# Kernel tuning notes

Hardware: AMD Instinct MI355X
Metric: run time of the kernel (lower is better)

The kernel has to match this reference:

```python
import jax, jax.numpy as jnp
import numpy as np
from jax import lax

TAGSET_SIZE = 64
START_TAG = TAGSET_SIZE - 2
STOP_TAG = TAGSET_SIZE - 1
NEG_INF = -10000.0


def setup_inputs() -> dict:
    key = jax.random.key(0)
    k_feat, k_trans, k_tags = jax.random.split(key, 3)
    B, S, T = 512, 1024, TAGSET_SIZE
    feats = jax.random.normal(k_feat, (B, S, T), dtype=jnp.float32)
    transitions = jax.random.normal(k_trans, (T, T), dtype=jnp.float32)
    # CRF constraints: nothing transitions FROM anything into START row semantics
    # of the torch code: transitions[START, :] = -1e4 ; transitions[:, STOP] = -1e4
    transitions = transitions.at[START_TAG, :].set(NEG_INF)
    transitions = transitions.at[:, STOP_TAG].set(NEG_INF)
    tags = jax.random.randint(k_tags, (B, S), 0, T - 2, dtype=jnp.int64)
    mask = jnp.ones((B, S), dtype=jnp.int32)
    return {"feats": feats, "transitions": transitions, "tags": tags, "mask": mask}


def _forward_alg(feats, transitions, maskf):
    # feats: (B,S,T), maskf: (B,S) float
    B, S, T = feats.shape
    init = jnp.full((B, T), NEG_INF, dtype=feats.dtype).at[:, START_TAG].set(0.0)

    def step(fv, xs):
        feat, m = xs  # feat: (B,T), m: (B,)
        # next_tag_var[b, next, prev] = fv[b,prev] + trans[next,prev] + feat[b,next]
        nxt = jax.nn.logsumexp(
            fv[:, None, :] + transitions[None, :, :] + feat[:, :, None], axis=2
        )
        m1 = m[:, None]
        return nxt * m1 + fv * (1.0 - m1), None

    fv, _ = lax.scan(step, init, (feats.transpose(1, 0, 2), maskf.T))
    terminal = fv + transitions[STOP_TAG][None, :]
    return jax.nn.logsumexp(terminal, axis=1)  # (B,)


def _score_sentence(feats, transitions, tags, maskf):
    B, S, T = feats.shape
    tags_ext = jnp.concatenate(
        [jnp.full((B, 1), START_TAG, dtype=tags.dtype), tags], axis=1
    )  # (B, S+1)
    cur = tags_ext[:, 1:]   # (B,S)
    prev = tags_ext[:, :-1]  # (B,S)
    emit = jnp.take_along_axis(feats, cur[:, :, None], axis=2)[:, :, 0]  # (B,S)
    trans = transitions[cur, prev]  # (B,S)
    score = jnp.sum((emit + trans) * maskf, axis=1)
    last_idx = maskf.sum(axis=1).astype(jnp.int32)  # index into tags_ext
    last_tags = jnp.take_along_axis(tags_ext, last_idx[:, None].astype(tags.dtype), axis=1)[:, 0]
    return score + transitions[STOP_TAG, last_tags]


def reference(feats, transitions, tags, mask):
    maskf = mask.astype(feats.dtype)
    forward_score = _forward_alg(feats, transitions, maskf)
    gold_score = _score_sentence(feats, transitions, tags, maskf)
    return jnp.mean(forward_score - gold_score)
```

## Files before the change

### kernel.cpp

```cpp
#include <hip/hip_runtime.h>

#define START_TAG 62
#define STOP_TAG 63
#define BATCH 512
#define SLEN 1024
#define NG 32
#define NCHAIN 64
#define RD 12
#define AH 8
#define SLOTB 4096
#define RINGB (RD * SLOTB)

typedef float vf4 __attribute__((ext_vector_type(4)));
typedef short short8 __attribute__((ext_vector_type(8)));

__device__ __forceinline__ unsigned pk_bf16(float lo, float hi) {
  return __builtin_amdgcn_perm(__float_as_uint(hi), __float_as_uint(lo), 0x07060302u);
}
__device__ __forceinline__ short bf16_rne(float x) {
  unsigned u = __float_as_uint(x);
  u += 0x7FFFu + ((u >> 16) & 1u);
  return (short)(u >> 16);
}
__device__ __forceinline__ vf4 mfma16(short8 a, short8 b, vf4 c) {
  return __builtin_amdgcn_mfma_f32_16x16x32_bf16(a, b, c, 0, 0, 0);
}
__device__ __forceinline__ void async16(const void* g, void* l) {
  __builtin_amdgcn_global_load_lds((const __attribute__((address_space(1))) unsigned*)g,
                                   (__attribute__((address_space(3))) unsigned*)l, 16, 0, 0);
}

template<int DIR, bool MASKED>
__device__ __forceinline__ void chain_run(const float* __restrict__ feats,
                                          const float* __restrict__ trans,
                                          const int* __restrict__ mask,
                                          float* __restrict__ ws, char* smem, int g) {
  const int lane = threadIdx.x & 63;
  const int q = lane >> 4, col = lane & 15;
  const int b = g * 16 + col;

  short8 A[4][2];
  const int mrow = 16 * (col >> 2) + (col & 3);
  #pragma unroll
  for (int t = 0; t < 4; ++t) {
    #pragma unroll
    for (int c = 0; c < 2; ++c) {
      short8 a;
      #pragma unroll
      for (int j = 0; j < 8; ++j) {
        int R = mrow + 4 * t, K = 16 * q + 8 * c + j;
        float tv = (DIR == 0) ? trans[R * 64 + K] : trans[K * 64 + R];
        a[j] = bf16_rne(__expf(tv));
      }
      A[t][c] = a;
    }
  }

  float W[16];
  float C = 0.f;
  if (DIR == 0) {
    #pragma unroll
    for (int i = 0; i < 16; ++i) W[i] = 0.f;
    if (q == 3) W[14] = 1.f;
  } else {
    #pragma unroll
    for (int i = 0; i < 16; ++i) W[i] = __expf(trans[STOP_TAG * 64 + 16 * q + i]);
  }

  const char* gb = (const char*)feats + (size_t)b * 262144 + (size_t)q * 64;

  vf4 cur[4];
  int rOff = 0, wOff = 0;
  if constexpr (!MASKED) {
    asm volatile("s_waitcnt vmcnt(0)" ::: "memory");
    #pragma unroll
    for (int p = 0; p < AH; ++p) {
      int s = (DIR == 0) ? p : 1023 - p;
      #pragma unroll
      for (int v = 0; v < 4; ++v)
        async16(gb + (size_t)s * 256 + v * 16, smem + p * SLOTB + v * 1024);
    }
    wOff = AH * SLOTB;
    asm volatile("s_waitcnt vmcnt(28)" ::: "memory");
    #pragma unroll
    for (int v = 0; v < 4; ++v)
      cur[v] = *(const vf4*)(smem + v * 1024 + lane * 16);
    rOff = SLOTB;
  } else {
    int s0 = (DIR == 0) ? 0 : 1023;
    #pragma unroll
    for (int v = 0; v < 4; ++v)
      cur[v] = *(const vf4*)(gb + (size_t)s0 * 256 + v * 16);
  }

  for (int grp = 0; grp < 128; ++grp) {
    #pragma unroll
    for (int u = 0; u < 4; ++u) {
      const int j = grp * 4 + u;
      float e[16];
      #pragma unroll
      for (int v = 0; v < 4; ++v)
        #pragma unroll
        for (int i = 0; i < 4; ++i) e[v * 4 + i] = __expf(cur[v][i]);

      float P[16];
      #pragma unroll
      for (int i = 0; i < 16; ++i) P[i] = (DIR == 0) ? W[i] : W[i] * e[i];

      union { unsigned uu[4]; short8 s8; } B0, B1;
      B0.uu[0] = pk_bf16(P[0], P[1]);   B0.uu[1] = pk_bf16(P[2], P[3]);
      B0.uu[2] = pk_bf16(P[4], P[5]);   B0.uu[3] = pk_bf16(P[6], P[7]);
      B1.uu[0] = pk_bf16(P[8], P[9]);   B1.uu[1] = pk_bf16(P[10], P[11]);
      B1.uu[2] = pk_bf16(P[12], P[13]); B1.uu[3] = pk_bf16(P[14], P[15]);

      vf4 z4 = {0.f, 0.f, 0.f, 0.f};
      vf4 d0 = mfma16(A[0][0], B0.s8, z4);
      vf4 d1 = mfma16(A[1][0], B0.s8, z4);
      vf4 d2 = mfma16(A[2][0], B0.s8, z4);
      vf4 d3 = mfma16(A[3][0], B0.s8, z4);
      d0 = mfma16(A[0][1], B1.s8, d0);
      d1 = mfma16(A[1][1], B1.s8, d1);
      d2 = mfma16(A[2][1], B1.s8, d2);
      d3 = mfma16(A[3][1], B1.s8, d3);

      int m = 1;
      if constexpr (!MASKED) {
        asm volatile("s_waitcnt vmcnt(24)" ::: "memory");
        #pragma unroll
        for (int v = 0; v < 4; ++v)
          cur[v] = *(const vf4*)(smem + rOff + v * 1024 + lane * 16);
        rOff += SLOTB; if (rOff == RINGB) rOff = 0;
        int jp = j + AH; if (jp > 511) jp = 511;
        int sp = (DIR == 0) ? jp : 1023 - jp;
        #pragma unroll
        for (int v = 0; v < 4; ++v)
          async16(gb + (size_t)sp * 256 + v * 16, smem + wOff + v * 1024);
        wOff += SLOTB; if (wOff == RINGB) wOff = 0;
      } else {
        int sj = (DIR == 0) ? j : 1023 - j;
        m = mask[b * 1024 + sj];
        int sn = (DIR == 0) ? (j + 1) : 1023 - (j + 1);
        #pragma unroll
        for (int v = 0; v < 4; ++v)
          cur[v] = *(const vf4*)(gb + (size_t)sn * 256 + v * 16);
      }

      #pragma unroll
      for (int i = 0; i < 4; ++i) {
        float n0 = (DIR == 0) ? d0[i] * e[i]      : d0[i];
        float n1 = (DIR == 0) ? d1[i] * e[4 + i]  : d1[i];
        float n2 = (DIR == 0) ? d2[i] * e[8 + i]  : d2[i];
        float n3 = (DIR == 0) ? d3[i] * e[12 + i] : d3[i];
        if (MASKED) {
          W[i]      = m ? n0 : W[i];
          W[4 + i]  = m ? n1 : W[4 + i];
          W[8 + i]  = m ? n2 : W[8 + i];
          W[12 + i] = m ? n3 : W[12 + i];
        } else {
          W[i] = n0; W[4 + i] = n1; W[8 + i] = n2; W[12 + i] = n3;
        }
      }
    }
    float z = __shfl(W[0], col);
    float rz = __builtin_amdgcn_rcpf(z);
    C += __logf(z);
    #pragma unroll
    for (int i = 0; i < 16; ++i) W[i] *= rz;
  }

  float* slab = ws + (size_t)(g * 2 + DIR) * 1024;
  #pragma unroll
  for (int t4 = 0; t4 < 4; ++t4) {
    vf4 o = {W[t4 * 4], W[t4 * 4 + 1], W[t4 * 4 + 2], W[t4 * 4 + 3]};
    *(vf4*)(slab + lane * 16 + t4 * 4) = o;
  }
  if (q == 0) ws[65536 + (g * 2 + DIR) * 16 + col] = C;
}

__global__ __launch_bounds__(64, 1)
void crf_main(const float* __restrict__ feats, const float* __restrict__ trans,
              const int* __restrict__ tags, const int* __restrict__ mask,
              float* __restrict__ ws) {
  __shared__ char smem[RINGB];
  const int blk = blockIdx.x;
  if (blk < NCHAIN) {
    const int g = blk >> 1, dir = blk & 1;
    const int lane = threadIdx.x & 63;
    const int q = lane >> 4, col = lane & 15;
    const int b = g * 16 + col;
    const int sB = dir ? 512 : 0;
    int anyz = 0;
    for (int it = 0; it < 32; ++it) {
      int4 v = *(const int4*)(mask + b * 1024 + sB + (it * 4 + q) * 4);
      anyz |= (v.x == 0) | (v.y == 0) | (v.z == 0) | (v.w == 0);
    }
    bool allones = (__ballot(anyz != 0) == 0ull);
    if (allones) {
      if (dir == 0) chain_run<0, false>(feats, trans, mask, ws, smem, g);
      else          chain_run<1, false>(feats, trans, mask, ws, smem, g);
    } else {
      if (dir == 0) chain_run<0, true>(feats, trans, mask, ws, smem, g);
      else          chain_run<1, true>(feats, trans, mask, ws, smem, g);
    }
    (void)tags;
  } else {
    const int b = blk - NCHAIN;
    const int* tb = tags + b * SLEN;
    const int* mb = mask + b * SLEN;
    const float* fbg = feats + (size_t)b * 65536;
    float acc = 0.f, cnt = 0.f;
    const int t = threadIdx.x;
    for (int k = 0; k < 16; ++k) {
      int s = t + k * 64;
      int cur = tb[s];
      int prev = (s == 0) ? START_TAG : tb[s - 1];
      float m = (float)mb[s];
      acc += m * (fbg[s * 64 + cur] + trans[cur * 64 + prev]);
      cnt += m;
    }
    #pragma unroll
    for (int o = 1; o < 64; o <<= 1) {
      acc += __shfl_xor(acc, o);
      cnt += __shfl_xor(cnt, o);
    }
    if (t == 0) {
      int last_idx = (int)(cnt + 0.5f);
      int last_tag = (last_idx == 0) ? START_TAG : tb[last_idx - 1];
      ws[66560 + b] = acc + trans[STOP_TAG * 64 + last_tag];
    }
  }
}

__global__ __launch_bounds__(512)
void crf_reduce(const float* __restrict__ ws, float* __restrict__ out) {
  __shared__ float s[512];
  const int t = threadIdx.x;
  const int g = t >> 4, col = t & 15;
  const float* Wf = ws + (size_t)(2 * g) * 1024;
  const float* Wb = ws + (size_t)(2 * g + 1) * 1024;
  float P = 0.f;
  #pragma unroll
  for (int q = 0; q < 4; ++q)
    #pragma unroll
    for (int i = 0; i < 16; ++i)
      P += Wf[(q * 16 + col) * 16 + i] * Wb[(q * 16 + col) * 16 + i];
  float sc = ws[65536 + (2 * g) * 16 + col] + ws[65536 + (2 * g + 1) * 16 + col] + __logf(P);
  s[t] = sc - ws[66560 + t];
  __syncthreads();
  for (int off = 256; off > 0; off >>= 1) {
    if (t < off) s[t] += s[t + off];
    __syncthreads();
  }
  if (t == 0) out[0] = s[0] * (1.f / 512.f);
}

extern "C" void kernel_launch(void* const* d_in, const int* in_sizes, int n_in,
                              void* d_out, int out_size, void* d_ws, size_t ws_size,
                              hipStream_t stream) {
  const float* feats = (const float*)d_in[0];
  const float* trans = (const float*)d_in[1];
  const int* tags = (const int*)d_in[2];
  const int* mask = (const int*)d_in[3];
  float* ws = (float*)d_ws;
  float* out = (float*)d_out;

  crf_main<<<NCHAIN + BATCH, 64, 0, stream>>>(feats, trans, tags, mask, ws);
  crf_reduce<<<1, 512, 0, stream>>>(ws, out);
}
```

Before: 309.6 us.

## Restructure fast CRF chain with 16-slot ring, compile-time slots, deferred renormalization

Splits the chain kernel into separate unmasked-fast and masked paths. The fast path now uses a 16-slot LDS ring, which lets a 16-step unrolled loop use compile-time slot indices instead of runtime offset arithmetic. Each async prefetch is issued before its matching wait, and the next step's LDS read happens early. Renormalization runs every 4 steps using a scale value captured one interval earlier, which takes the cross-lane shuffle off the critical dependency chain. The cost is more LDS per block and a deferred scale that lets values grow slightly more between rescales.

```diff
diff --git a/kernel.cpp b/kernel.cpp
--- a/kernel.cpp
+++ b/kernel.cpp
@@ -4,12 +4,10 @@
 #define STOP_TAG 63
 #define BATCH 512
 #define SLEN 1024
-#define NG 32
 #define NCHAIN 64
-#define RD 12
+#define RD 16
 #define AH 8
 #define SLOTB 4096
-#define RINGB (RD * SLOTB)
 
 typedef float vf4 __attribute__((ext_vector_type(4)));
 typedef short short8 __attribute__((ext_vector_type(8)));
@@ -30,16 +28,9 @@
                                    (__attribute__((address_space(3))) unsigned*)l, 16, 0, 0);
 }
 
-template<int DIR, bool MASKED>
-__device__ __forceinline__ void chain_run(const float* __restrict__ feats,
-                                          const float* __restrict__ trans,
-                                          const int* __restrict__ mask,
-                                          float* __restrict__ ws, char* smem, int g) {
-  const int lane = threadIdx.x & 63;
-  const int q = lane >> 4, col = lane & 15;
-  const int b = g * 16 + col;
-
-  short8 A[4][2];
+template<int DIR>
+__device__ __forceinline__ void load_A(const float* __restrict__ trans, short8 A[4][2],
+                                       int q, int col) {
   const int mrow = 16 * (col >> 2) + (col & 3);
   #pragma unroll
   for (int t = 0; t < 4; ++t) {
@@ -55,9 +46,32 @@
       A[t][c] = a;
     }
   }
+}
+
+template<int DIR>
+__device__ __forceinline__ void epilogue(float* __restrict__ ws, const float W[16],
+                                         float C, int g, int lane, int q, int col) {
+  float* slab = ws + (size_t)(g * 2 + DIR) * 1024;
+  #pragma unroll
+  for (int t4 = 0; t4 < 4; ++t4) {
+    vf4 o = {W[t4 * 4], W[t4 * 4 + 1], W[t4 * 4 + 2], W[t4 * 4 + 3]};
+    *(vf4*)(slab + lane * 16 + t4 * 4) = o;
+  }
+  if (q == 0) ws[65536 + (g * 2 + DIR) * 16 + col] = C;
+}
+
+template<int DIR>
+__device__ __forceinline__ void chain_fast(const float* __restrict__ feats,
+                                           const float* __restrict__ trans,
+                                           float* __restrict__ ws, char* smem, int g) {
+  const int lane = threadIdx.x & 63;
+  const int q = lane >> 4, col = lane & 15;
+  const int b = g * 16 + col;
+
+  short8 A[4][2];
+  load_A<DIR>(trans, A, q, col);
 
   float W[16];
-  float C = 0.f;
   if (DIR == 0) {
     #pragma unroll
     for (int i = 0; i < 16; ++i) W[i] = 0.f;
@@ -69,34 +83,39 @@
 
   const char* gb = (const char*)feats + (size_t)b * 262144 + (size_t)q * 64;
 
+  asm volatile("s_waitcnt vmcnt(0)" ::: "memory");
+  #pragma unroll
+  for (int p = 0; p < AH; ++p) {
+    size_t s = (DIR == 0) ? (size_t)p : (size_t)(1023 - p);
+    #pragma unroll
+    for (int v = 0; v < 4; ++v)
+      async16(gb + s * 256 + v * 16, smem + p * SLOTB + v * 1024);
+  }
+  asm volatile("s_waitcnt vmcnt(28)" ::: "memory");
   vf4 cur[4];
-  int rOff = 0, wOff = 0;
-  if constexpr (!MASKED) {
-    asm volatile("s_waitcnt vmcnt(0)" ::: "memory");
-    #pragma unroll
-    for (int p = 0; p < AH; ++p) {
-      int s = (DIR == 0) ? p : 1023 - p;
-      #pragma unroll
-      for (int v = 0; v < 4; ++v)
-        async16(gb + (size_t)s * 256 + v * 16, smem + p * SLOTB + v * 1024);
-    }
-    wOff = AH * SLOTB;
-    asm volatile("s_waitcnt vmcnt(28)" ::: "memory");
-    #pragma unroll
-    for (int v = 0; v < 4; ++v)
-      cur[v] = *(const vf4*)(smem + v * 1024 + lane * 16);
-    rOff = SLOTB;
-  } else {
-    int s0 = (DIR == 0) ? 0 : 1023;
-    #pragma unroll
-    for (int v = 0; v < 4; ++v)
-      cur[v] = *(const vf4*)(gb + (size_t)s0 * 256 + v * 16);
-  }
-
-  for (int grp = 0; grp < 128; ++grp) {
-    #pragma unroll
-    for (int u = 0; u < 4; ++u) {
-      const int j = grp * 4 + u;
+  #pragma unroll
+  for (int v = 0; v < 4; ++v)
+    cur[v] = *(const vf4*)(smem + v * 1024 + lane * 16);
+
+  float C = 0.f, zpend = 1.f;
+
+  for (int bk = 0; bk < 32; ++bk) {
+    #pragma unroll
+    for (int u = 0; u < 16; ++u) {
+      const int j = bk * 16 + u;
+      int jp = j + AH; if (jp > 511) jp = 511;
+      const size_t sp = (DIR == 0) ? (size_t)jp : (size_t)(1023 - jp);
+      const int wslot = (u + AH) & 15;
+      #pragma unroll
+      for (int v = 0; v < 4; ++v)
+        async16(gb + sp * 256 + v * 16, smem + wslot * SLOTB + v * 1024);
+      asm volatile("s_waitcnt vmcnt(28)" ::: "memory");
+      const int rslot = (u + 1) & 15;
+      vf4 nxt[4];
+      #pragma unroll
+      for (int v = 0; v < 4; ++v)
+        nxt[v] = *(const vf4*)(smem + rslot * SLOTB + v * 1024 + lane * 16);
+
       float e[16];
       #pragma unroll
       for (int v = 0; v < 4; ++v)
@@ -123,27 +142,96 @@
       d2 = mfma16(A[2][1], B1.s8, d2);
       d3 = mfma16(A[3][1], B1.s8, d3);
 
-      int m = 1;
-      if constexpr (!MASKED) {
-        asm volatile("s_waitcnt vmcnt(24)" ::: "memory");
+      #pragma unroll
+      for (int i = 0; i < 4; ++i) {
+        W[i]      = (DIR == 0) ? d0[i] * e[i]      : d0[i];
+        W[4 + i]  = (DIR == 0) ? d1[i] * e[4 + i]  : d1[i];
+        W[8 + i]  = (DIR == 0) ? d2[i] * e[8 + i]  : d2[i];
+        W[12 + i] = (DIR == 0) ? d3[i] * e[12 + i] : d3[i];
+      }
+      #pragma unroll
+      for (int v = 0; v < 4; ++v) cur[v] = nxt[v];
+
+      if ((u & 3) == 3) {
+        float rz = __builtin_amdgcn_rcpf(zpend);
+        C += __logf(zpend);
         #pragma unroll
-        for (int v = 0; v < 4; ++v)
-          cur[v] = *(const vf4*)(smem + rOff + v * 1024 + lane * 16);
-        rOff += SLOTB; if (rOff == RINGB) rOff = 0;
-        int jp = j + AH; if (jp > 511) jp = 511;
-        int sp = (DIR == 0) ? jp : 1023 - jp;
+        for (int i = 0; i < 16; ++i) W[i] *= rz;
+        zpend = __shfl(W[0], col);
+      }
+    }
+  }
+  epilogue<DIR>(ws, W, C, g, lane, q, col);
+}
+
+template<int DIR>
+__device__ __forceinline__ void chain_masked(const float* __restrict__ feats,
+                                             const float* __restrict__ trans,
+                                             const int* __restrict__ mask,
+                                             float* __restrict__ ws, int g) {
+  const int lane = threadIdx.x & 63;
+  const int q = lane >> 4, col = lane & 15;
+  const int b = g * 16 + col;
+
+  short8 A[4][2];
+  load_A<DIR>(trans, A, q, col);
+
+  float W[16];
+  float C = 0.f;
+  if (DIR == 0) {
+    #pragma unroll
+    for (int i = 0; i < 16; ++i) W[i] = 0.f;
+    if (q == 3) W[14] = 1.f;
+  } else {
+    #pragma unroll
+    for (int i = 0; i < 16; ++i) W[i] = __expf(trans[STOP_TAG * 64 + 16 * q + i]);
+  }
+
+  const char* gb = (const char*)feats + (size_t)b * 262144 + (size_t)q * 64;
+  vf4 cur[4];
+  {
+    size_t s0 = (DIR == 0) ? 0 : 1023;
+    #pragma unroll
+    for (int v = 0; v < 4; ++v)
+      cur[v] = *(const vf4*)(gb + s0 * 256 + (size_t)v * 16);
+  }
+
+  for (int grp = 0; grp < 128; ++grp) {
+    #pragma unroll
+    for (int u = 0; u < 4; ++u) {
+      const int j = grp * 4 + u;
+      float e[16];
+      #pragma unroll
+      for (int v = 0; v < 4; ++v)
         #pragma unroll
-        for (int v = 0; v < 4; ++v)
-          async16(gb + (size_t)sp * 256 + v * 16, smem + wOff + v * 1024);
-        wOff += SLOTB; if (wOff == RINGB) wOff = 0;
-      } else {
-        int sj = (DIR == 0) ? j : 1023 - j;
-        m = mask[b * 1024 + sj];
-        int sn = (DIR == 0) ? (j + 1) : 1023 - (j + 1);
-        #pragma unroll
-        for (int v = 0; v < 4; ++v)
-          cur[v] = *(const vf4*)(gb + (size_t)sn * 256 + v * 16);
-      }
+        for (int i = 0; i < 4; ++i) e[v * 4 + i] = __expf(cur[v][i]);
+
+      float P[16];
+      #pragma unroll
+      for (int i = 0; i < 16; ++i) P[i] = (DIR == 0) ? W[i] : W[i] * e[i];
+
+      union { unsigned uu[4]; short8 s8; } B0, B1;
+      B0.uu[0] = pk_bf16(P[0], P[1]);   B0.uu[1] = pk_bf16(P[2], P[3]);
+      B0.uu[2] = pk_bf16(P[4], P[5]);   B0.uu[3] = pk_bf16(P[6], P[7]);
+      B1.uu[0] = pk_bf16(P[8], P[9]);   B1.uu[1] = pk_bf16(P[10], P[11]);
+      B1.uu[2] = pk_bf16(P[12], P[13]); B1.uu[3] = pk_bf16(P[14], P[15]);
+
+      vf4 z4 = {0.f, 0.f, 0.f, 0.f};
+      vf4 d0 = mfma16(A[0][0], B0.s8, z4);
+      vf4 d1 = mfma16(A[1][0], B0.s8, z4);
+      vf4 d2 = mfma16(A[2][0], B0.s8, z4);
+      vf4 d3 = mfma16(A[3][0], B0.s8, z4);
+      d0 = mfma16(A[0][1], B1.s8, d0);
+      d1 = mfma16(A[1][1], B1.s8, d1);
+      d2 = mfma16(A[2][1], B1.s8, d2);
+      d3 = mfma16(A[3][1], B1.s8, d3);
+
+      int sj = (DIR == 0) ? j : 1023 - j;
+      int m = mask[b * 1024 + sj];
+      int sn = (DIR == 0) ? (j + 1) : 1023 - (j + 1);
+      #pragma unroll
+      for (int v = 0; v < 4; ++v)
+        cur[v] = *(const vf4*)(gb + (size_t)sn * 256 + (size_t)v * 16);
 
       #pragma unroll
       for (int i = 0; i < 4; ++i) {
@@ -151,14 +239,10 @@
         float n1 = (DIR == 0) ? d1[i] * e[4 + i]  : d1[i];
         float n2 = (DIR == 0) ? d2[i] * e[8 + i]  : d2[i];
         float n3 = (DIR == 0) ? d3[i] * e[12 + i] : d3[i];
-        if (MASKED) {
-          W[i]      = m ? n0 : W[i];
-          W[4 + i]  = m ? n1 : W[4 + i];
-          W[8 + i]  = m ? n2 : W[8 + i];
-          W[12 + i] = m ? n3 : W[12 + i];
-        } else {
-          W[i] = n0; W[4 + i] = n1; W[8 + i] = n2; W[12 + i] = n3;
-        }
+        W[i]      = m ? n0 : W[i];
+        W[4 + i]  = m ? n1 : W[4 + i];
+        W[8 + i]  = m ? n2 : W[8 + i];
+        W[12 + i] = m ? n3 : W[12 + i];
       }
     }
     float z = __shfl(W[0], col);
@@ -167,21 +251,14 @@
     #pragma unroll
     for (int i = 0; i < 16; ++i) W[i] *= rz;
   }
-
-  float* slab = ws + (size_t)(g * 2 + DIR) * 1024;
-  #pragma unroll
-  for (int t4 = 0; t4 < 4; ++t4) {
-    vf4 o = {W[t4 * 4], W[t4 * 4 + 1], W[t4 * 4 + 2], W[t4 * 4 + 3]};
-    *(vf4*)(slab + lane * 16 + t4 * 4) = o;
-  }
-  if (q == 0) ws[65536 + (g * 2 + DIR) * 16 + col] = C;
+  epilogue<DIR>(ws, W, C, g, lane, q, col);
 }
 
 __global__ __launch_bounds__(64, 1)
 void crf_main(const float* __restrict__ feats, const float* __restrict__ trans,
               const int* __restrict__ tags, const int* __restrict__ mask,
               float* __restrict__ ws) {
-  __shared__ char smem[RINGB];
+  __shared__ char smem[RD * SLOTB];
   const int blk = blockIdx.x;
   if (blk < NCHAIN) {
     const int g = blk >> 1, dir = blk & 1;
@@ -196,11 +273,11 @@
     }
     bool allones = (__ballot(anyz != 0) == 0ull);
     if (allones) {
-      if (dir == 0) chain_run<0, false>(feats, trans, mask, ws, smem, g);
-      else          chain_run<1, false>(feats, trans, mask, ws, smem, g);
+      if (dir == 0) chain_fast<0>(feats, trans, ws, smem, g);
+      else          chain_fast<1>(feats, trans, ws, smem, g);
     } else {
-      if (dir == 0) chain_run<0, true>(feats, trans, mask, ws, smem, g);
-      else          chain_run<1, true>(feats, trans, mask, ws, smem, g);
+      if (dir == 0) chain_masked<0>(feats, trans, mask, ws, g);
+      else          chain_masked<1>(feats, trans, mask, ws, g);
     }
     (void)tags;
   } else {
```

After: 301.6 us. 2.6% less time.
